# Optimization experiments

Hardware: AMD Instinct MI355X
Metric: run time of the kernel (lower is better)

Reference implementation:

```python
import jax, jax.numpy as jnp
import numpy as np

COMMITMENT_COST = 0.25


def setup_inputs() -> dict:
    key = jax.random.key(0)
    k1, k2 = jax.random.split(key)
    z = jax.random.normal(k1, (4096, 512), dtype=jnp.float32)
    # stacked codebooks: [num_codebooks, codebook_size, latent_dim]
    codebooks = jax.random.normal(k2, (8, 16384, 512), dtype=jnp.float32)
    return {"z": z, "codebooks": codebooks}


def reference(z, codebooks):
    """Residual VQ forward. Returns (quantized [B,D], loss scalar, indices [B,K])."""
    z_sg = jax.lax.stop_gradient(z)

    def step(carry, cb):
        residual, quantized, loss = carry
        # squared L2 distances: [B, C]
        d = (jnp.sum(residual * residual, axis=1, keepdims=True)
             + jnp.sum(cb * cb, axis=1)
             - 2.0 * (residual @ cb.T))
        idx = jnp.argmin(d, axis=1)              # [B]
        q_i = cb[idx]                            # gather: [B, D]
        commitment = COMMITMENT_COST * jnp.mean((jax.lax.stop_gradient(q_i) - z) ** 2)
        codebook_l = jnp.mean((q_i - z_sg) ** 2)
        loss = loss + commitment + codebook_l
        return (residual - q_i, quantized + q_i, loss), idx

    init = (z, jnp.zeros_like(z), jnp.float32(0.0))
    (_, quantized, loss), idxs = jax.lax.scan(step, init, codebooks)
    return quantized, loss, idxs.T  # indices: [B, num_codebooks]
```

## Files before the change

### kernel.cpp

```cpp
#include <hip/hip_runtime.h>

typedef _Float16 half8 __attribute__((ext_vector_type(8)));
typedef _Float16 half4v __attribute__((ext_vector_type(4)));
typedef float f32x4 __attribute__((ext_vector_type(4)));

#define MFMA_F16 __builtin_amdgcn_mfma_f32_16x16x32_f16

static constexpr int BATCH  = 4096;
static constexpr int DIM    = 512;
static constexpr int CODES  = 16384;
static constexpr int NCB    = 8;
static constexpr int NCHUNK = 8;
static constexpr int CHUNK  = CODES / NCHUNK;
static constexpr int NT     = CHUNK / 16;
static constexpr int HTILES = NT / 2;
static constexpr int BM     = 128;
static constexpr int NPC    = NCHUNK * 2 * 2;
static constexpr int TILE_H = 8192;
static constexpr int TILE_B = 16384;
static constexpr float LO_SCALE = 2048.0f;
static constexpr float LO_INV   = 1.0f / 2048.0f;
static constexpr float DELTA    = 0.25f;

__device__ __forceinline__ int swz(int code, int kk) {
  return code * DIM + (kk ^ (((code ^ (kk >> 6)) & 7) << 3));
}

__global__ __launch_bounds__(256) void k_init(const float* __restrict__ z,
                                              float* __restrict__ resid,
                                              _Float16* __restrict__ rhi,
                                              _Float16* __restrict__ rlo) {
  int i = blockIdx.x * 256 + threadIdx.x;
  float4 v = ((const float4*)z)[i];
  ((float4*)resid)[i] = v;
  half4v h, l;
  const float* vf = (const float*)&v;
#pragma unroll
  for (int j = 0; j < 4; ++j) {
    float x = vf[j];
    _Float16 hi = (_Float16)x;
    h[j] = hi;
    l[j] = (_Float16)((x - (float)hi) * LO_SCALE);
  }
  *(half4v*)&rhi[(size_t)i * 4] = h;
  *(half4v*)&rlo[(size_t)i * 4] = l;
}

__global__ __launch_bounds__(256) void k_cnorm(const float* __restrict__ cb,
                                               float* __restrict__ cnorm) {
  int wave = threadIdx.x >> 6, lane = threadIdx.x & 63;
  int code = blockIdx.x * 4 + wave;
  const float4* src = (const float4*)(cb + (size_t)code * DIM);
  double s = 0.0;
#pragma unroll
  for (int j = 0; j < 2; ++j) {
    float4 v = src[lane * 2 + j];
    s += (double)v.x * v.x + (double)v.y * v.y + (double)v.z * v.z + (double)v.w * v.w;
  }
#pragma unroll
  for (int off = 32; off; off >>= 1) s += __shfl_down(s, off);
  if (lane == 0) cnorm[code] = (float)s;
}

__global__ __launch_bounds__(256) void k_cvtn(const float* __restrict__ cb,
                                              _Float16* __restrict__ dst,
                                              float* __restrict__ cnorm_k) {
  const int wave  = threadIdx.x >> 6;
  const int lane  = threadIdx.x & 63;
  const int chunk = blockIdx.x & 7;
  const int cidx  = (blockIdx.x >> 3) * 4 + wave;
  const int ntile = cidx >> 4;
  const int code  = cidx & 15;
  const int code_g = chunk * CHUNK + cidx;

  const float* src = cb + (size_t)code_g * DIM + lane * 8;
  float4 v0 = *(const float4*)src;
  float4 v1 = *(const float4*)(src + 4);
  half8 h;
  const float* f0 = (const float*)&v0;
  const float* f1 = (const float*)&v1;
  double s = 0.0;
#pragma unroll
  for (int e = 0; e < 4; ++e) {
    float x = f0[e];
    h[e] = (_Float16)x;
    s += (double)x * x;
    x = f1[e];
    h[e + 4] = (_Float16)x;
    s += (double)x * x;
  }
  const int pos = (lane >> 2) * 512 + (lane & 3) * 128 + code * 8;
  *(half8*)(dst + (size_t)(chunk * NT + ntile) * TILE_H + pos) = h;

#pragma unroll
  for (int off = 32; off; off >>= 1) s += __shfl_down(s, off);
  if (lane == 0) cnorm_k[code_g] = (float)s;
}

#define LEXLT(av, ai, bv, bi) ((av) < (bv) || ((av) == (bv) && (ai) < (bi)))

__global__ __launch_bounds__(256, 2) void k_argmin_pc(
    const _Float16* __restrict__ rhi,
    const _Float16* __restrict__ cvt,
    const float* __restrict__ cnorm,
    float* __restrict__ partmin, int* __restrict__ partidx) {
  const int tid   = threadIdx.x;
  const int lane  = tid & 63;
  const int wave  = tid >> 6;
  const int chunk = blockIdx.x & 7;
  const int idx   = blockIdx.x >> 3;
  const int mtile = idx >> 1;
  const int half  = idx & 1;
  const int nt0   = half * HTILES;
  const int cbase = chunk * CHUNK;
  const char* ctile = (const char*)(cvt + (size_t)chunk * NT * TILE_H);

  const int kb = (lane >> 4) * 8;
  half8 ah[2][16];
#pragma unroll
  for (int j = 0; j < 2; ++j) {
    const size_t rbase =
        (size_t)(mtile * BM + (2 * wave + j) * 16 + (lane & 15)) * DIM;
#pragma unroll
    for (int t = 0; t < 16; ++t)
      ah[j][t] = *(const half8*)(rhi + rbase + t * 32 + kb);
  }

  const int lbase = lane * 16;
  const int rcode = lane & 15;

  float tv0[2][4], tv1[2][4];
  int   ti0[2][4], ti1[2][4];
#pragma unroll
  for (int j = 0; j < 2; ++j)
#pragma unroll
    for (int r = 0; r < 4; ++r) {
      tv0[j][r] = tv1[j][r] = 3.4e38f;
      ti0[j][r] = ti1[j][r] = 0x7fffffff;
    }

  half8 s0[4], s1[4];

#define LOAD_Q(S, NTI, Q)                                                    \
  {                                                                          \
    const char* bp_ = ctile + (size_t)(NTI) * TILE_B + (Q) * 4096 + lbase;   \
    S[0] = *(const half8*)(bp_);                                             \
    S[1] = *(const half8*)(bp_ + 1024);                                      \
    S[2] = *(const half8*)(bp_ + 2048);                                      \
    S[3] = *(const half8*)(bp_ + 3072);                                      \
  }

#define MFMA_Q(S, TB, AI)                                                    \
  {                                                                          \
    __builtin_amdgcn_s_setprio(1);                                           \
    _Pragma("unroll")                                                        \
    for (int j_ = 0; j_ < 4; ++j_) {                                         \
      _Pragma("unroll")                                                      \
      for (int b_ = 0; b_ < 2; ++b_)                                         \
        acc[b_][AI] = MFMA_F16(ah[b_][(TB) + j_], S[j_], acc[b_][AI], 0, 0, 0); \
    }                                                                        \
    __builtin_amdgcn_s_setprio(0);                                           \
  }

#define TOP2_INS(d, cg, J, R)                                                \
  {                                                                          \
    bool b0_ = (d) < tv0[J][R];                                              \
    bool b1_ = (d) < tv1[J][R];                                              \
    tv1[J][R] = b0_ ? tv0[J][R] : (b1_ ? (d) : tv1[J][R]);                   \
    ti1[J][R] = b0_ ? ti0[J][R] : (b1_ ? (cg) : ti1[J][R]);                  \
    tv0[J][R] = b0_ ? (d) : tv0[J][R];                                       \
    ti0[J][R] = b0_ ? (cg) : ti0[J][R];                                      \
  }

  LOAD_Q(s0, nt0, 0);
  float cn_cur = cnorm[cbase + nt0 * 16 + rcode];

  for (int it = 0; it < HTILES; ++it) {
    const int nt = nt0 + it;
    const bool more = (it + 1 < HTILES);
    float cn_next = more ? cnorm[cbase + (nt + 1) * 16 + rcode] : 0.f;

    f32x4 acc[2][2];
#pragma unroll
    for (int b = 0; b < 2; ++b) {
      acc[b][0] = (f32x4){0.f, 0.f, 0.f, 0.f};
      acc[b][1] = (f32x4){0.f, 0.f, 0.f, 0.f};
    }

    LOAD_Q(s1, nt, 1);
    MFMA_Q(s0, 0, 0);
    LOAD_Q(s0, nt, 2);
    MFMA_Q(s1, 4, 1);
    LOAD_Q(s1, nt, 3);
    MFMA_Q(s0, 8, 0);
    const int pn = more ? nt + 1 : nt;
    LOAD_Q(s0, pn, 0);
    MFMA_Q(s1, 12, 1);

    const int codeg = cbase + nt * 16 + rcode;
#pragma unroll
    for (int j = 0; j < 2; ++j) {
      f32x4 dh = acc[j][0] + acc[j][1];
#pragma unroll
      for (int r = 0; r < 4; ++r) {
        float d = cn_cur - 2.0f * dh[r];
        TOP2_INS(d, codeg, j, r);
      }
    }
    cn_cur = cn_next;
  }
#undef LOAD_Q
#undef MFMA_Q
#undef TOP2_INS

#pragma unroll
  for (int s = 1; s < 16; s <<= 1) {
#pragma unroll
    for (int j = 0; j < 2; ++j) {
#pragma unroll
      for (int r = 0; r < 4; ++r) {
        float b0v = __shfl_xor(tv0[j][r], s), b1v = __shfl_xor(tv1[j][r], s);
        int   b0i = __shfl_xor(ti0[j][r], s), b1i = __shfl_xor(ti1[j][r], s);
        bool p0 = LEXLT(tv0[j][r], ti0[j][r], b0v, b0i);
        float r0v = p0 ? tv0[j][r] : b0v;  int r0i = p0 ? ti0[j][r] : b0i;
        float xv  = p0 ? b0v : tv0[j][r];  int xi  = p0 ? b0i : ti0[j][r];
        bool p1 = LEXLT(tv1[j][r], ti1[j][r], b1v, b1i);
        float yv = p1 ? tv1[j][r] : b1v;   int yi = p1 ? ti1[j][r] : b1i;
        bool p2 = LEXLT(xv, xi, yv, yi);
        float r1v = p2 ? xv : yv;          int r1i = p2 ? xi : yi;
        tv0[j][r] = r0v; ti0[j][r] = r0i;
        tv1[j][r] = r1v; ti1[j][r] = r1i;
      }
    }
  }
  if ((lane & 15) == 0) {
    const int pslot = chunk * 2 + half;
#pragma unroll
    for (int j = 0; j < 2; ++j) {
      const int rowbase = mtile * BM + (2 * wave + j) * 16 + (lane >> 4) * 4;
#pragma unroll
      for (int r = 0; r < 4; ++r) {
        const size_t base = (size_t)(rowbase + r) * NPC + pslot * 2;
        partmin[base + 0] = tv0[j][r]; partidx[base + 0] = ti0[j][r];
        partmin[base + 1] = tv1[j][r]; partidx[base + 1] = ti1[j][r];
      }
    }
  }
}

__device__ __forceinline__ void load8(const float* __restrict__ cb, int cbase, int nt,
                                      int s_code, int s_kseg, float4 v[8]) {
  const float4* src = (const float4*)(cb + (size_t)(cbase + nt * 16 + s_code) * DIM + s_kseg);
#pragma unroll
  for (int j = 0; j < 8; ++j) v[j] = src[j];
}

__device__ __forceinline__ void cvt_store(_Float16* __restrict__ BHbuf,
                                          _Float16* __restrict__ BLbuf,
                                          int code, int kseg, const float4 sv[8]) {
  const float* f = (const float*)sv;
#pragma unroll
  for (int j = 0; j < 4; ++j) {
    half8 h, l;
#pragma unroll
    for (int e = 0; e < 8; ++e) {
      float x = f[j * 8 + e];
      _Float16 hi = (_Float16)x;
      h[e] = hi;
      l[e] = (_Float16)((x - (float)hi) * LO_SCALE);
    }
    int hw = swz(code, kseg + j * 8);
    *(half8*)(BHbuf + hw) = h;
    *(half8*)(BLbuf + hw) = l;
  }
}

__global__ __launch_bounds__(256, 2) void k_argmin_fb(
    const _Float16* __restrict__ rhi, const _Float16* __restrict__ rlo,
    const float* __restrict__ cb, const float* __restrict__ cnorm,
    float* __restrict__ partmin, int* __restrict__ partidx) {
  __shared__ _Float16 BH[2][16 * DIM];
  __shared__ _Float16 BL[2][16 * DIM];
  __shared__ float CN[CHUNK];

  const int tid   = threadIdx.x;
  const int lane  = tid & 63;
  const int wave  = tid >> 6;
  const int mtile = blockIdx.x >> 3;
  const int chunk = blockIdx.x & 7;
  const int cbase = chunk * CHUNK;

  {
    const float4* s = (const float4*)(cnorm + cbase);
    float4* d = (float4*)CN;
    for (int i = tid; i < CHUNK / 4; i += 256) d[i] = s[i];
  }

  const int arow = mtile * 64 + wave * 16 + (lane & 15);
  const int kb = (lane >> 4) * 8;
  half8 ah[16], al[16];
#pragma unroll
  for (int t = 0; t < 16; ++t) {
    ah[t] = *(const half8*)(rhi + (size_t)arow * DIM + t * 32 + kb);
    al[t] = *(const half8*)(rlo + (size_t)arow * DIM + t * 32 + kb);
  }

  const int s_code = tid >> 4;
  const int s_kseg = (tid & 15) * 32;

  float rmin[4] = {3.4e38f, 3.4e38f, 3.4e38f, 3.4e38f};
  int   ridx[4] = {0, 0, 0, 0};

  {
    float4 v0[8];
    load8(cb, cbase, 0, s_code, s_kseg, v0);
    cvt_store(&BH[0][0], &BL[0][0], s_code, s_kseg, v0);
  }

  const int rcode = lane & 15;
  for (int nt = 0; nt < NT; ++nt) {
    __syncthreads();
    const int cur = nt & 1;
    const bool more = (nt + 1 < NT);
    float4 nv[8];
    if (more) load8(cb, cbase, nt + 1, s_code, s_kseg, nv);

    f32x4 acch  = {0.f, 0.f, 0.f, 0.f};
    f32x4 accl0 = {0.f, 0.f, 0.f, 0.f};
    f32x4 accl1 = {0.f, 0.f, 0.f, 0.f};
    const _Float16* bh = &BH[cur][0];
    const _Float16* bl = &BL[cur][0];
#pragma unroll
    for (int t = 0; t < 16; ++t) {
      const int hw = swz(rcode, t * 32 + kb);
      half8 fbh = *(const half8*)(bh + hw);
      half8 fbl = *(const half8*)(bl + hw);
      acch  = MFMA_F16(ah[t], fbh, acch, 0, 0, 0);
      accl0 = MFMA_F16(ah[t], fbl, accl0, 0, 0, 0);
      accl1 = MFMA_F16(al[t], fbh, accl1, 0, 0, 0);
    }
    float cn = CN[nt * 16 + rcode];
    int codeg = cbase + nt * 16 + rcode;
#pragma unroll
    for (int r = 0; r < 4; ++r) {
      float d = cn - 2.0f * (acch[r] + (accl0[r] + accl1[r]) * LO_INV);
      if (d < rmin[r]) { rmin[r] = d; ridx[r] = codeg; }
    }
    if (more) cvt_store(&BH[cur ^ 1][0], &BL[cur ^ 1][0], s_code, s_kseg, nv);
  }

#pragma unroll
  for (int s = 1; s < 16; s <<= 1) {
#pragma unroll
    for (int r = 0; r < 4; ++r) {
      float ov = __shfl_xor(rmin[r], s);
      int   oi = __shfl_xor(ridx[r], s);
      if (ov < rmin[r] || (ov == rmin[r] && oi < ridx[r])) { rmin[r] = ov; ridx[r] = oi; }
    }
  }
  if ((lane & 15) == 0) {
    int rowbase = mtile * 64 + wave * 16 + (lane >> 4) * 4;
#pragma unroll
    for (int r = 0; r < 4; ++r) {
#pragma unroll
      for (int t = 0; t < 4; ++t) {
        partmin[(size_t)(rowbase + r) * NPC + chunk * 4 + t] = rmin[r];
        partidx[(size_t)(rowbase + r) * NPC + chunk * 4 + t] = ridx[r];
      }
    }
  }
}

__global__ __launch_bounds__(256) void k_update(
    const float* __restrict__ cb, const float* __restrict__ z,
    const float* __restrict__ partmin, const int* __restrict__ partidx,
    float* __restrict__ resid, _Float16* __restrict__ rhi, _Float16* __restrict__ rlo,
    float* __restrict__ quant, float* __restrict__ out_idx,
    float* __restrict__ losspart, int step) {
  __shared__ int   s_idx[16];
  __shared__ int   s_cand[16][32];
  __shared__ int   s_cnt[16];
  __shared__ float s_red[4];
  const int tid = threadIdx.x;
  const int row0 = blockIdx.x * 16;

  if (tid < 16) {
    const int row = row0 + tid;
    float m = 3.4e38f;
    for (int c = 0; c < NPC; ++c) {
      float v = partmin[(size_t)row * NPC + c];
      if (v < m) m = v;
    }
    int cnt = 0;
    for (int c = 0; c < NPC; ++c) {
      float v = partmin[(size_t)row * NPC + c];
      if (v < m + DELTA) s_cand[tid][cnt++] = partidx[(size_t)row * NPC + c];
    }
    s_cnt[tid] = cnt;
  }
  __syncthreads();

  {
    const int wv = tid >> 6, ln = tid & 63;
    for (int rr = wv; rr < 16; rr += 4) {
      const int row = row0 + rr;
      const float* rrow = resid + (size_t)row * DIM + ln * 8;
      double bestd = 1.0e300;
      int    besti = 0x7fffffff;
      const int cnt = s_cnt[rr];
      for (int c = 0; c < cnt; ++c) {
        const int ci = s_cand[rr][c];
        const float* crow = cb + (size_t)ci * DIM + ln * 8;
        double s = 0.0;
#pragma unroll
        for (int e = 0; e < 8; ++e) {
          double df = (double)rrow[e] - (double)crow[e];
          s += df * df;
        }
#pragma unroll
        for (int off = 32; off; off >>= 1) s += __shfl_down(s, off);
        s = __shfl(s, 0);
        if (s < bestd || (s == bestd && ci < besti)) { bestd = s; besti = ci; }
      }
      if (ln == 0) {
        s_idx[rr] = besti;
        out_idx[(size_t)row * NCB + step] = (float)besti;
      }
    }
  }
  __syncthreads();

  float lsum = 0.f;
  const int sub = tid >> 7;
  const int e   = tid & 127;
  for (int rp = 0; rp < 16; rp += 2) {
    const int rl = rp + sub;
    const int row = row0 + rl;
    const int idx = s_idx[rl];
    float4 q  = ((const float4*)cb)[(size_t)idx * 128 + e];
    float4 zv = ((const float4*)z)[(size_t)row * 128 + e];
    float4 rv = ((const float4*)resid)[(size_t)row * 128 + e];
    float4 nr, qa;
    const float* qf = (const float*)&q;
    const float* zf = (const float*)&zv;
    const float* rf = (const float*)&rv;
    float* nf = (float*)&nr;
    float* af = (float*)&qa;
    if (step == 0) {
#pragma unroll
      for (int j = 0; j < 4; ++j) af[j] = qf[j];
    } else {
      float4 old = ((const float4*)quant)[(size_t)row * 128 + e];
      const float* of = (const float*)&old;
#pragma unroll
      for (int j = 0; j < 4; ++j) af[j] = of[j] + qf[j];
    }
    ((float4*)quant)[(size_t)row * 128 + e] = qa;
    half4v h, l;
#pragma unroll
    for (int j = 0; j < 4; ++j) {
      float nrj = rf[j] - qf[j];
      nf[j] = nrj;
      _Float16 hi = (_Float16)nrj;
      h[j] = hi;
      l[j] = (_Float16)((nrj - (float)hi) * LO_SCALE);
      float dq = qf[j] - zf[j];
      lsum += dq * dq;
    }
    ((float4*)resid)[(size_t)row * 128 + e] = nr;
    *(half4v*)&rhi[(size_t)row * DIM + e * 4] = h;
    *(half4v*)&rlo[(size_t)row * DIM + e * 4] = l;
  }
#pragma unroll
  for (int off = 32; off; off >>= 1) lsum += __shfl_down(lsum, off);
  if ((tid & 63) == 0) s_red[tid >> 6] = lsum;
  __syncthreads();
  if (tid == 0) losspart[blockIdx.x] = s_red[0] + s_red[1] + s_red[2] + s_red[3];
}

__global__ __launch_bounds__(256) void k_loss(const float* __restrict__ losspart,
                                              float* __restrict__ out_loss) {
  __shared__ double red[4];
  const int tid = threadIdx.x;
  double s = 0.0;
  for (int i = tid; i < NCB * 256; i += 256) s += (double)losspart[i];
#pragma unroll
  for (int off = 32; off; off >>= 1) s += __shfl_down(s, off);
  if ((tid & 63) == 0) red[tid >> 6] = s;
  __syncthreads();
  if (tid == 0)
    out_loss[0] = (float)((red[0] + red[1] + red[2] + red[3]) *
                          (1.25 / (double)((size_t)BATCH * DIM)));
}

extern "C" void kernel_launch(void* const* d_in, const int* in_sizes, int n_in,
                              void* d_out, int out_size, void* d_ws, size_t ws_size,
                              hipStream_t stream) {
  const float* z  = (const float*)d_in[0];
  const float* cb = (const float*)d_in[1];
  float* out = (float*)d_out;
  float* quant    = out;
  float* out_loss = out + (size_t)BATCH * DIM;
  float* out_idx  = out + (size_t)BATCH * DIM + 1;

  char* ws = (char*)d_ws;
  float*    resid    = (float*)ws;
  _Float16* rhi      = (_Float16*)(ws + ((size_t)8  << 20));
  _Float16* rlo      = (_Float16*)(ws + ((size_t)12 << 20));
  float*    cnorm    = (float*)(ws + ((size_t)16 << 20));
  float*    partmin  = (float*)(ws + ((size_t)17 << 20));
  int*      partidx  = (int*)  (ws + ((size_t)18 << 20));
  float*    losspart = (float*)(ws + ((size_t)19 << 20));
  _Float16* cvtbuf   = (_Float16*)(ws + ((size_t)20 << 20));

  const size_t REQ = ((size_t)20 << 20) + ((size_t)16 << 20);
  const bool pre = (ws_size >= REQ);

  k_init<<<dim3((BATCH * DIM / 4) / 256), dim3(256), 0, stream>>>(z, resid, rhi, rlo);
  if (!pre)
    k_cnorm<<<dim3(NCB * CODES / 4), dim3(256), 0, stream>>>(cb, cnorm);

  for (int k = 0; k < NCB; ++k) {
    const float* cbk = cb + (size_t)k * CODES * DIM;
    if (pre) {
      k_cvtn<<<dim3(CODES * 64 / 256), dim3(256), 0, stream>>>(
          cbk, cvtbuf, cnorm + (size_t)k * CODES);
      k_argmin_pc<<<dim3((BATCH / BM) * NCHUNK * 2), dim3(256), 0, stream>>>(
          rhi, cvtbuf, cnorm + (size_t)k * CODES, partmin, partidx);
    } else {
      k_argmin_fb<<<dim3((BATCH / 64) * NCHUNK), dim3(256), 0, stream>>>(
          rhi, rlo, cbk, cnorm + (size_t)k * CODES, partmin, partidx);
    }
    k_update<<<dim3(BATCH / 16), dim3(256), 0, stream>>>(
        cbk, z, partmin, partidx, resid, rhi, rlo,
        quant, out_idx, losspart + k * 256, k);
  }
  k_loss<<<dim3(1), dim3(256), 0, stream>>>(losspart, out_loss);
}
```

Measured before the change: 933.8 us.

## Fuse next-codebook conversion into update kernel with double-buffered fp16 image

```diff
diff --git a/kernel.cpp b/kernel.cpp
--- a/kernel.cpp
+++ b/kernel.cpp
@@ -18,12 +18,67 @@
 static constexpr int NPC    = NCHUNK * 2 * 2;
 static constexpr int TILE_H = 8192;
 static constexpr int TILE_B = 16384;
+static constexpr size_t CBIMG_H = (size_t)NCHUNK * NT * TILE_H;
 static constexpr float LO_SCALE = 2048.0f;
 static constexpr float LO_INV   = 1.0f / 2048.0f;
 static constexpr float DELTA    = 0.25f;
 
 __device__ __forceinline__ int swz(int code, int kk) {
   return code * DIM + (kk ^ (((code ^ (kk >> 6)) & 7) << 3));
+}
+
+__device__ __forceinline__ void cvt_one(const float* __restrict__ cbsrc,
+                                        _Float16* __restrict__ img,
+                                        float* __restrict__ cnorm_k,
+                                        int bid, int wave, int lane) {
+  const int chunk = bid & 7;
+  const int cidx  = (bid >> 3) * 4 + wave;
+  const int ntile = cidx >> 4;
+  const int code  = cidx & 15;
+  const int code_g = chunk * CHUNK + cidx;
+
+  const float* src = cbsrc + (size_t)code_g * DIM + lane * 8;
+  float4 v0 = *(const float4*)src;
+  float4 v1 = *(const float4*)(src + 4);
+  half8 h;
+  const float* f0 = (const float*)&v0;
+  const float* f1 = (const float*)&v1;
+  double s = 0.0;
+#pragma unroll
+  for (int e = 0; e < 4; ++e) {
+    float x = f0[e];
+    h[e] = (_Float16)x;
+    s += (double)x * x;
+    x = f1[e];
+    h[e + 4] = (_Float16)x;
+    s += (double)x * x;
+  }
+  const int pos = (lane >> 2) * 512 + (lane & 3) * 128 + code * 8;
+  *(half8*)(img + (size_t)(chunk * NT + ntile) * TILE_H + pos) = h;
+
+#pragma unroll
+  for (int off = 32; off; off >>= 1) s += __shfl_down(s, off);
+  if (lane == 0) cnorm_k[code_g] = (float)s;
+}
+
+__global__ __launch_bounds__(256) void k_initcvt(const float* __restrict__ z,
+                                                 float* __restrict__ resid,
+                                                 _Float16* __restrict__ rhi,
+                                                 const float* __restrict__ cb0,
+                                                 _Float16* __restrict__ img0,
+                                                 float* __restrict__ cnorm0) {
+  if (blockIdx.x < 2048) {
+    int i = blockIdx.x * 256 + threadIdx.x;
+    float4 v = ((const float4*)z)[i];
+    ((float4*)resid)[i] = v;
+    half4v h;
+    const float* vf = (const float*)&v;
+#pragma unroll
+    for (int j = 0; j < 4; ++j) h[j] = (_Float16)vf[j];
+    *(half4v*)&rhi[(size_t)i * 4] = h;
+  } else {
+    cvt_one(cb0, img0, cnorm0, blockIdx.x - 2048, threadIdx.x >> 6, threadIdx.x & 63);
+  }
 }
 
 __global__ __launch_bounds__(256) void k_init(const float* __restrict__ z,
@@ -60,41 +115,6 @@
 #pragma unroll
   for (int off = 32; off; off >>= 1) s += __shfl_down(s, off);
   if (lane == 0) cnorm[code] = (float)s;
-}
-
-__global__ __launch_bounds__(256) void k_cvtn(const float* __restrict__ cb,
-                                              _Float16* __restrict__ dst,
-                                              float* __restrict__ cnorm_k) {
-  const int wave  = threadIdx.x >> 6;
-  const int lane  = threadIdx.x & 63;
-  const int chunk = blockIdx.x & 7;
-  const int cidx  = (blockIdx.x >> 3) * 4 + wave;
-  const int ntile = cidx >> 4;
-  const int code  = cidx & 15;
-  const int code_g = chunk * CHUNK + cidx;
-
-  const float* src = cb + (size_t)code_g * DIM + lane * 8;
-  float4 v0 = *(const float4*)src;
-  float4 v1 = *(const float4*)(src + 4);
-  half8 h;
-  const float* f0 = (const float*)&v0;
-  const float* f1 = (const float*)&v1;
-  double s = 0.0;
-#pragma unroll
-  for (int e = 0; e < 4; ++e) {
-    float x = f0[e];
-    h[e] = (_Float16)x;
-    s += (double)x * x;
-    x = f1[e];
-    h[e + 4] = (_Float16)x;
-    s += (double)x * x;
-  }
-  const int pos = (lane >> 2) * 512 + (lane & 3) * 128 + code * 8;
-  *(half8*)(dst + (size_t)(chunk * NT + ntile) * TILE_H + pos) = h;
-
-#pragma unroll
-  for (int off = 32; off; off >>= 1) s += __shfl_down(s, off);
-  if (lane == 0) cnorm_k[code_g] = (float)s;
 }
 
 #define LEXLT(av, ai, bv, bi) ((av) < (bv) || ((av) == (bv) && (ai) < (bi)))
@@ -371,18 +391,18 @@
   }
 }
 
-__global__ __launch_bounds__(256) void k_update(
+__device__ __forceinline__ void update_role(
     const float* __restrict__ cb, const float* __restrict__ z,
     const float* __restrict__ partmin, const int* __restrict__ partidx,
     float* __restrict__ resid, _Float16* __restrict__ rhi, _Float16* __restrict__ rlo,
     float* __restrict__ quant, float* __restrict__ out_idx,
-    float* __restrict__ losspart, int step) {
+    float* __restrict__ losspart, int step, int blk) {
   __shared__ int   s_idx[16];
   __shared__ int   s_cand[16][32];
   __shared__ int   s_cnt[16];
   __shared__ float s_red[4];
   const int tid = threadIdx.x;
-  const int row0 = blockIdx.x * 16;
+  const int row0 = blk * 16;
 
   if (tid < 16) {
     const int row = row0 + tid;
@@ -469,13 +489,39 @@
     }
     ((float4*)resid)[(size_t)row * 128 + e] = nr;
     *(half4v*)&rhi[(size_t)row * DIM + e * 4] = h;
-    *(half4v*)&rlo[(size_t)row * DIM + e * 4] = l;
+    if (rlo) *(half4v*)&rlo[(size_t)row * DIM + e * 4] = l;
   }
 #pragma unroll
   for (int off = 32; off; off >>= 1) lsum += __shfl_down(lsum, off);
   if ((tid & 63) == 0) s_red[tid >> 6] = lsum;
   __syncthreads();
-  if (tid == 0) losspart[blockIdx.x] = s_red[0] + s_red[1] + s_red[2] + s_red[3];
+  if (tid == 0) losspart[blk] = s_red[0] + s_red[1] + s_red[2] + s_red[3];
+}
+
+__global__ __launch_bounds__(256) void k_upcvt(
+    const float* __restrict__ cbk, const float* __restrict__ z,
+    const float* __restrict__ partmin, const int* __restrict__ partidx,
+    float* __restrict__ resid, _Float16* __restrict__ rhi,
+    float* __restrict__ quant, float* __restrict__ out_idx,
+    float* __restrict__ losspart, int step,
+    const float* __restrict__ cbn, _Float16* __restrict__ imgn,
+    float* __restrict__ cnormn) {
+  if (blockIdx.x < 256) {
+    update_role(cbk, z, partmin, partidx, resid, rhi, nullptr,
+                quant, out_idx, losspart, step, blockIdx.x);
+  } else {
+    cvt_one(cbn, imgn, cnormn, blockIdx.x - 256, threadIdx.x >> 6, threadIdx.x & 63);
+  }
+}
+
+__global__ __launch_bounds__(256) void k_update(
+    const float* __restrict__ cb, const float* __restrict__ z,
+    const float* __restrict__ partmin, const int* __restrict__ partidx,
+    float* __restrict__ resid, _Float16* __restrict__ rhi, _Float16* __restrict__ rlo,
+    float* __restrict__ quant, float* __restrict__ out_idx,
+    float* __restrict__ losspart, int step) {
+  update_role(cb, z, partmin, partidx, resid, rhi, rlo,
+              quant, out_idx, losspart, step, blockIdx.x);
 }
 
 __global__ __launch_bounds__(256) void k_loss(const float* __restrict__ losspart,
@@ -511,29 +557,45 @@
   float*    partmin  = (float*)(ws + ((size_t)17 << 20));
   int*      partidx  = (int*)  (ws + ((size_t)18 << 20));
   float*    losspart = (float*)(ws + ((size_t)19 << 20));
-  _Float16* cvtbuf   = (_Float16*)(ws + ((size_t)20 << 20));
-
-  const size_t REQ = ((size_t)20 << 20) + ((size_t)16 << 20);
+  _Float16* cvtbuf0  = (_Float16*)(ws + ((size_t)20 << 20));
+  _Float16* cvtbuf1  = (_Float16*)(ws + ((size_t)36 << 20));
+
+  const size_t REQ = ((size_t)36 << 20) + ((size_t)16 << 20);
   const bool pre = (ws_size >= REQ);
 
-  k_init<<<dim3((BATCH * DIM / 4) / 256), dim3(256), 0, stream>>>(z, resid, rhi, rlo);
-  if (!pre)
+  if (pre) {
+    k_initcvt<<<dim3(2048 + 4096), dim3(256), 0, stream>>>(
+        z, resid, rhi, cb, cvtbuf0, cnorm);
+
+    for (int k = 0; k < NCB; ++k) {
+      const float* cbk = cb + (size_t)k * CODES * DIM;
+      _Float16* imgk = (k & 1) ? cvtbuf1 : cvtbuf0;
+      k_argmin_pc<<<dim3((BATCH / BM) * NCHUNK * 2), dim3(256), 0, stream>>>(
+          rhi, imgk, cnorm + (size_t)k * CODES, partmin, partidx);
+      if (k + 1 < NCB) {
+        const float* cbn = cb + (size_t)(k + 1) * CODES * DIM;
+        _Float16* imgn = ((k + 1) & 1) ? cvtbuf1 : cvtbuf0;
+        k_upcvt<<<dim3(256 + 4096), dim3(256), 0, stream>>>(
+            cbk, z, partmin, partidx, resid, rhi,
+            quant, out_idx, losspart + k * 256, k,
+            cbn, imgn, cnorm + (size_t)(k + 1) * CODES);
+      } else {
+        k_update<<<dim3(BATCH / 16), dim3(256), 0, stream>>>(
+            cbk, z, partmin, partidx, resid, rhi, nullptr,
+            quant, out_idx, losspart + k * 256, k);
+      }
+    }
+  } else {
+    k_init<<<dim3((BATCH * DIM / 4) / 256), dim3(256), 0, stream>>>(z, resid, rhi, rlo);
     k_cnorm<<<dim3(NCB * CODES / 4), dim3(256), 0, stream>>>(cb, cnorm);
-
-  for (int k = 0; k < NCB; ++k) {
-    const float* cbk = cb + (size_t)k * CODES * DIM;
-    if (pre) {
-      k_cvtn<<<dim3(CODES * 64 / 256), dim3(256), 0, stream>>>(
-          cbk, cvtbuf, cnorm + (size_t)k * CODES);
-      k_argmin_pc<<<dim3((BATCH / BM) * NCHUNK * 2), dim3(256), 0, stream>>>(
-          rhi, cvtbuf, cnorm + (size_t)k * CODES, partmin, partidx);
-    } else {
+    for (int k = 0; k < NCB; ++k) {
+      const float* cbk = cb + (size_t)k * CODES * DIM;
       k_argmin_fb<<<dim3((BATCH / 64) * NCHUNK), dim3(256), 0, stream>>>(
           rhi, rlo, cbk, cnorm + (size_t)k * CODES, partmin, partidx);
-    }
-    k_update<<<dim3(BATCH / 16), dim3(256), 0, stream>>>(
-        cbk, z, partmin, partidx, resid, rhi, rlo,
-        quant, out_idx, losspart + k * 256, k);
+      k_update<<<dim3(BATCH / 16), dim3(256), 0, stream>>>(
+          cbk, z, partmin, partidx, resid, rhi, rlo,
+          quant, out_idx, losspart + k * 256, k);
+    }
   }
   k_loss<<<dim3(1), dim3(256), 0, stream>>>(losspart, out_loss);
 }
```

New measurement: 889.0 us. -4.8%, faster.
